# Performance work log

Hardware: AMD Instinct MI355X
Metric: run time of the kernel (lower is better)

Reference implementation:

```python
import jax, jax.numpy as jnp
import numpy as np

B, T, D, S, H = 1024, 365, 5, 27, 256


def setup_inputs() -> dict:
    key = jax.random.key(0)
    ks = jax.random.split(key, 12)
    sc = 0.05
    return {
        "x_dyn": jax.random.normal(ks[0], (B, T, D), dtype=jnp.float32),
        "x_stat": jax.random.normal(ks[1], (B, S), dtype=jnp.float32),
        "W_i": jax.random.normal(ks[2], (H, S), dtype=jnp.float32) * sc,
        "b_i": jnp.zeros((H,), dtype=jnp.float32),
        "W_f": jax.random.normal(ks[3], (H, D + H), dtype=jnp.float32) * sc,
        "b_f": jnp.zeros((H,), dtype=jnp.float32),
        "W_g": jax.random.normal(ks[4], (H, D + H), dtype=jnp.float32) * sc,
        "b_g": jnp.zeros((H,), dtype=jnp.float32),
        "W_o": jax.random.normal(ks[5], (H, D + H), dtype=jnp.float32) * sc,
        "b_o": jnp.zeros((H,), dtype=jnp.float32),
        "W_head": jax.random.normal(ks[6], (1, H), dtype=jnp.float32) * sc,
        "b_head": jnp.zeros((1,), dtype=jnp.float32),
    }


def _ealstm(x_dyn, x_stat, W_i, b_i, W_f, b_f, W_g, b_g, W_o, b_o, W_head, b_head):
    d = x_dyn.shape[-1]
    # static input gate (computed once, constant over time)
    i_gate = jax.nn.sigmoid(x_stat @ W_i.T + b_i)  # [B, H]
    # split concat-weights into dyn-input and hidden parts; precompute x projections
    W_fx, W_fh = W_f[:, :d], W_f[:, d:]
    W_gx, W_gh = W_g[:, :d], W_g[:, d:]
    W_ox, W_oh = W_o[:, :d], W_o[:, d:]
    pre_f = jnp.einsum("btd,hd->tbh", x_dyn, W_fx) + b_f  # [T, B, H]
    pre_g = jnp.einsum("btd,hd->tbh", x_dyn, W_gx) + b_g
    pre_o = jnp.einsum("btd,hd->tbh", x_dyn, W_ox) + b_o

    bsz = x_dyn.shape[0]
    h0 = jnp.zeros((bsz, W_f.shape[0]), dtype=x_dyn.dtype)
    c0 = jnp.zeros_like(h0)

    def step(carry, xs):
        h, c = carry
        pf, pg, po = xs
        f = jax.nn.sigmoid(pf + h @ W_fh.T)
        g = jnp.tanh(pg + h @ W_gh.T)
        o = jax.nn.sigmoid(po + h @ W_oh.T)
        c = f * c + i_gate * g
        h = o * jnp.tanh(c)
        return (h, c), None

    (h, _), _ = jax.lax.scan(step, (h0, c0), (pre_f, pre_g, pre_o))
    # dropout is identity in eval mode
    return h @ W_head.T + b_head  # [B, 1]


def reference(x_dyn, x_stat, W_i, b_i, W_f, b_f, W_g, b_g, W_o, b_o, W_head, b_head):
    return _ealstm(x_dyn, x_stat, W_i, b_i, W_f, b_f, W_g, b_g, W_o, b_o, W_head, b_head)
```

## Files before the change

kernel.cpp:

```cpp
#include <hip/hip_runtime.h>

#define HID      256
#define DDYN     5
#define NS       27
#define TS       365
#define BS       4
#define NW       8
#define UPW      32
#define NTILE    6
#define STRIDE_A 296
#define G3       768

typedef short short8 __attribute__((ext_vector_type(8)));
typedef float f32x4  __attribute__((ext_vector_type(4)));
typedef float f32x2  __attribute__((ext_vector_type(2)));

__device__ __forceinline__ unsigned short f2bf(float f) {
    union { float f; unsigned u; } v; v.f = f;
    unsigned r = v.u + 0x7FFFu + ((v.u >> 16) & 1u);
    return (unsigned short)(r >> 16);
}
__device__ __forceinline__ float fsig(float x) {
    float e = __builtin_amdgcn_exp2f(-1.4426950408889634f * x);
    return __builtin_amdgcn_rcpf(1.0f + e);
}
__device__ __forceinline__ float ftanh(float x) {
    float e = __builtin_amdgcn_exp2f(2.8853900817779268f * x);
    return 1.0f - 2.0f * __builtin_amdgcn_rcpf(1.0f + e);
}

__global__ __launch_bounds__(512, 2)
void ealstm_kernel(const float* __restrict__ x_dyn,  const float* __restrict__ x_stat,
                   const float* __restrict__ W_i,    const float* __restrict__ b_i,
                   const float* __restrict__ W_f,    const float* __restrict__ b_f,
                   const float* __restrict__ W_g,    const float* __restrict__ b_g,
                   const float* __restrict__ W_o,    const float* __restrict__ b_o,
                   const float* __restrict__ W_head, const float* __restrict__ b_head,
                   float* __restrict__ out)
{
    __shared__ __align__(16) unsigned short Abuf[2][16 * STRIDE_A];
    __shared__ __align__(16) float          pre[G3 * 4];
    __shared__ __align__(16) unsigned short WxL[G3 * 8];
    __shared__ __align__(16) unsigned short xc[TS * 20];
    __shared__ __align__(16) float          xst[BS * NS];

    const int tid  = threadIdx.x;
    const int bid  = blockIdx.x;
    const int b0   = bid * BS;
    const int lane = tid & 63;
    const int wv   = tid >> 6;
    const int q    = lane >> 4;
    const int n    = lane & 15;
    const int ul   = lane & 31;
    const int r0   = (lane >> 5) * 2;
    const int u    = wv * UPW + ul;

    for (int i = tid; i < 2 * 16 * STRIDE_A / 2; i += 512)
        ((unsigned int*)Abuf)[i] = 0u;
    for (int i = tid; i < BS * NS; i += 512)
        xst[i] = x_stat[(b0 + i / NS) * NS + (i % NS)];
    for (int i = tid; i < TS * BS * DDYN; i += 512) {
        int b  = i / (TS * DDYN);
        int rr = i - b * (TS * DDYN);
        int t  = rr / DDYN;
        int d  = rr - t * DDYN;
        xc[t * 20 + b * DDYN + d] =
            f2bf(x_dyn[(size_t)(b0 + b) * (TS * DDYN) + t * DDYN + d]);
    }
    for (int col = tid; col < G3; col += 512) {
        int gate = col >> 8, hc = col & 255;
        const float* Wg = gate == 0 ? W_f : (gate == 1 ? W_g : W_o);
        const float* bg = gate == 0 ? b_f : (gate == 1 ? b_g : b_o);
        #pragma unroll
        for (int d = 0; d < DDYN; d++) WxL[col * 8 + d] = f2bf(Wg[hc * (DDYN + HID) + d]);
        WxL[col * 8 + 5] = f2bf(bg[hc]);
        WxL[col * 8 + 6] = 0; WxL[col * 8 + 7] = 0;
    }
    __syncthreads();
    if (tid < 2 * BS) Abuf[tid >> 2][(tid & 3) * STRIDE_A + 261] = 0x3F80;
    if (tid < BS * DDYN) {
        int r = tid / DDYN, d = tid - r * DDYN;
        Abuf[0][r * STRIDE_A + 256 + d] = xc[r * DDYN + d];
    }

    short8 Bf[NTILE][8];
    #pragma unroll
    for (int j = 0; j < NTILE; j++) {
        int g = j >> 1;
        int urow = wv * UPW + (j & 1) * 16 + n;
        const float* Wg = g == 0 ? W_f : (g == 1 ? W_g : W_o);
        const float* wrow = Wg + urow * (DDYN + HID) + DDYN;
        #pragma unroll
        for (int c = 0; c < 8; c++) {
            int k0 = c * 32 + q * 8;
            short8 fr;
            #pragma unroll
            for (int e = 0; e < 8; e++) fr[e] = (short)f2bf(wrow[k0 + e]);
            Bf[j][c] = fr;
        }
    }

    float ig0, ig1, c0 = 0.f, c1 = 0.f, h0f = 0.f, h1f = 0.f;
    {
        float a0 = b_i[u], a1 = a0;
        for (int s = 0; s < NS; s++) {
            float w = W_i[u * NS + s];
            a0 += xst[r0 * NS + s] * w;
            a1 += xst[(r0 + 1) * NS + s] * w;
        }
        ig0 = fsig(a0); ig1 = fsig(a1);
    }
    const float whead = W_head[u];
    __syncthreads();

    const int aoff = n * STRIDE_A;
    const int pb   = (wv * 96 + ul) * 4 + r0;

    for (int t = 0; t < TS; t++) {
        const unsigned short* __restrict__ pA = Abuf[t & 1];
        unsigned short*       __restrict__ pB = Abuf[(t + 1) & 1];

        f32x4 acc[NTILE];
        #pragma unroll
        for (int j = 0; j < NTILE; j++) acc[j] = (f32x4){0.f, 0.f, 0.f, 0.f};
        #pragma unroll
        for (int c = 0; c < 8; c++) {
            short8 a = *(const short8*)&pA[aoff + c * 32 + q * 8];
            #pragma unroll
            for (int j = 0; j < NTILE; j++)
                acc[j] = __builtin_amdgcn_mfma_f32_16x16x32_bf16(a, Bf[j][c], acc[j], 0, 0, 0);
        }
        {
            short8 a8 = *(const short8*)&pA[aoff + 256 + q * 8];
            #pragma unroll
            for (int j = 0; j < NTILE; j++) {
                short8 b8 = {};
                if (q == 0) {
                    int col = (j >> 1) * 256 + wv * UPW + (j & 1) * 16 + n;
                    b8 = *(const short8*)&WxL[col * 8];
                }
                acc[j] = __builtin_amdgcn_mfma_f32_16x16x32_bf16(a8, b8, acc[j], 0, 0, 0);
            }
        }
        if (q == 0) {
            #pragma unroll
            for (int j = 0; j < NTILE; j++)
                *(f32x4*)&pre[(wv * 96 + (j >> 1) * 32 + (j & 1) * 16 + n) * 4] = acc[j];
        }
        __asm__ volatile("s_waitcnt lgkmcnt(0)" ::: "memory");

        f32x2 pf = *(const f32x2*)&pre[pb];
        f32x2 pg = *(const f32x2*)&pre[pb + 128];
        f32x2 po = *(const f32x2*)&pre[pb + 256];
        {
            float f  = fsig(pf[0]);
            float g_ = ftanh(pg[0]);
            float o  = fsig(po[0]);
            c0 = f * c0 + ig0 * g_;
            float h = o * ftanh(c0);
            pB[r0 * STRIDE_A + u] = f2bf(h);
            if (t == TS - 1) h0f = h;
        }
        {
            float f  = fsig(pf[1]);
            float g_ = ftanh(pg[1]);
            float o  = fsig(po[1]);
            c1 = f * c1 + ig1 * g_;
            float h = o * ftanh(c1);
            pB[(r0 + 1) * STRIDE_A + u] = f2bf(h);
            if (t == TS - 1) h1f = h;
        }
        if (t + 1 < TS && tid < BS * DDYN) {
            int r = tid / DDYN, d = tid - r * DDYN;
            pB[r * STRIDE_A + 256 + d] = xc[(t + 1) * 20 + tid];
        }
        __syncthreads();
    }

    pre[u * 4 + r0]     = h0f * whead;
    pre[u * 4 + r0 + 1] = h1f * whead;
    __syncthreads();
    if (tid < 64) {
        f32x4 s = *(const f32x4*)&pre[tid * 4];
        #pragma unroll
        for (int k = 1; k < 4; k++) {
            f32x4 v = *(const f32x4*)&pre[(tid + k * 64) * 4];
            #pragma unroll
            for (int r = 0; r < BS; r++) s[r] += v[r];
        }
        #pragma unroll
        for (int off = 32; off > 0; off >>= 1)
            #pragma unroll
            for (int r = 0; r < BS; r++) s[r] += __shfl_down(s[r], off, 64);
        if (tid == 0) {
            float bh = b_head[0];
            #pragma unroll
            for (int r = 0; r < BS; r++) out[b0 + r] = s[r] + bh;
        }
    }
}

extern "C" void kernel_launch(void* const* d_in, const int* in_sizes, int n_in,
                              void* d_out, int out_size, void* d_ws, size_t ws_size,
                              hipStream_t stream) {
    ealstm_kernel<<<256, 512, 0, stream>>>(
        (const float*)d_in[0],  (const float*)d_in[1],  (const float*)d_in[2],
        (const float*)d_in[3],  (const float*)d_in[4],  (const float*)d_in[5],
        (const float*)d_in[6],  (const float*)d_in[7],  (const float*)d_in[8],
        (const float*)d_in[9],  (const float*)d_in[10], (const float*)d_in[11],
        (float*)d_out);
}
```

Measured before the change: 707.9 us.

## Split LSTM recurrence across 16 waves with one unit-row per thread

Doubles the block to 1024 threads, so each of 16 waves owns 16 hidden units and 3 MFMA tiles instead of 32 units and 6 tiles. Each thread now updates a single (unit, batch-row) cell state. The aim is to shorten the serial per-timestep MFMA chain and gate math on the recurrence critical path. The cost is a barrier across 16 waves every step and tighter register limits per thread. The final hidden state is now read back from the bf16 shared buffer instead of being kept in fp32, a small precision change.

Measured after the change: 707.2 us. No clear change (-0.1%).

```diff
diff --git a/kernel.cpp b/kernel.cpp
--- a/kernel.cpp
+++ b/kernel.cpp
@@ -5,21 +5,24 @@
 #define NS       27
 #define TS       365
 #define BS       4
-#define NW       8
-#define UPW      32
-#define NTILE    6
+#define NW       16
+#define UPW      16
+#define NTILE    3
 #define STRIDE_A 296
 #define G3       768
 
 typedef short short8 __attribute__((ext_vector_type(8)));
 typedef float f32x4  __attribute__((ext_vector_type(4)));
-typedef float f32x2  __attribute__((ext_vector_type(2)));
 
 __device__ __forceinline__ unsigned short f2bf(float f) {
     union { float f; unsigned u; } v; v.f = f;
     unsigned r = v.u + 0x7FFFu + ((v.u >> 16) & 1u);
     return (unsigned short)(r >> 16);
 }
+__device__ __forceinline__ float bf2f(unsigned short s) {
+    union { unsigned u; float f; } v; v.u = ((unsigned)s) << 16;
+    return v.f;
+}
 __device__ __forceinline__ float fsig(float x) {
     float e = __builtin_amdgcn_exp2f(-1.4426950408889634f * x);
     return __builtin_amdgcn_rcpf(1.0f + e);
@@ -29,7 +32,7 @@
     return 1.0f - 2.0f * __builtin_amdgcn_rcpf(1.0f + e);
 }
 
-__global__ __launch_bounds__(512, 2)
+__global__ __launch_bounds__(1024)
 void ealstm_kernel(const float* __restrict__ x_dyn,  const float* __restrict__ x_stat,
                    const float* __restrict__ W_i,    const float* __restrict__ b_i,
                    const float* __restrict__ W_f,    const float* __restrict__ b_f,
@@ -39,7 +42,7 @@
                    float* __restrict__ out)
 {
     __shared__ __align__(16) unsigned short Abuf[2][16 * STRIDE_A];
-    __shared__ __align__(16) float          pre[G3 * 4];
+    __shared__ __align__(16) float          pre[NW * 192];
     __shared__ __align__(16) unsigned short WxL[G3 * 8];
     __shared__ __align__(16) unsigned short xc[TS * 20];
     __shared__ __align__(16) float          xst[BS * NS];
@@ -51,15 +54,15 @@
     const int wv   = tid >> 6;
     const int q    = lane >> 4;
     const int n    = lane & 15;
-    const int ul   = lane & 31;
-    const int r0   = (lane >> 5) * 2;
-    const int u    = wv * UPW + ul;
-
-    for (int i = tid; i < 2 * 16 * STRIDE_A / 2; i += 512)
+    const int up   = lane >> 2;
+    const int r    = lane & 3;
+    const int u    = wv * UPW + up;
+
+    for (int i = tid; i < 2 * 16 * STRIDE_A / 2; i += 1024)
         ((unsigned int*)Abuf)[i] = 0u;
-    for (int i = tid; i < BS * NS; i += 512)
+    for (int i = tid; i < BS * NS; i += 1024)
         xst[i] = x_stat[(b0 + i / NS) * NS + (i % NS)];
-    for (int i = tid; i < TS * BS * DDYN; i += 512) {
+    for (int i = tid; i < TS * BS * DDYN; i += 1024) {
         int b  = i / (TS * DDYN);
         int rr = i - b * (TS * DDYN);
         int t  = rr / DDYN;
@@ -67,7 +70,8 @@
         xc[t * 20 + b * DDYN + d] =
             f2bf(x_dyn[(size_t)(b0 + b) * (TS * DDYN) + t * DDYN + d]);
     }
-    for (int col = tid; col < G3; col += 512) {
+    if (tid < G3) {
+        int col = tid;
         int gate = col >> 8, hc = col & 255;
         const float* Wg = gate == 0 ? W_f : (gate == 1 ? W_g : W_o);
         const float* bg = gate == 0 ? b_f : (gate == 1 ? b_g : b_o);
@@ -79,16 +83,15 @@
     __syncthreads();
     if (tid < 2 * BS) Abuf[tid >> 2][(tid & 3) * STRIDE_A + 261] = 0x3F80;
     if (tid < BS * DDYN) {
-        int r = tid / DDYN, d = tid - r * DDYN;
-        Abuf[0][r * STRIDE_A + 256 + d] = xc[r * DDYN + d];
+        int rr = tid / DDYN, d = tid - rr * DDYN;
+        Abuf[0][rr * STRIDE_A + 256 + d] = xc[rr * DDYN + d];
     }
 
     short8 Bf[NTILE][8];
     #pragma unroll
     for (int j = 0; j < NTILE; j++) {
-        int g = j >> 1;
-        int urow = wv * UPW + (j & 1) * 16 + n;
-        const float* Wg = g == 0 ? W_f : (g == 1 ? W_g : W_o);
+        int urow = wv * UPW + n;
+        const float* Wg = j == 0 ? W_f : (j == 1 ? W_g : W_o);
         const float* wrow = Wg + urow * (DDYN + HID) + DDYN;
         #pragma unroll
         for (int c = 0; c < 8; c++) {
@@ -100,21 +103,17 @@
         }
     }
 
-    float ig0, ig1, c0 = 0.f, c1 = 0.f, h0f = 0.f, h1f = 0.f;
+    float ig, cst = 0.f;
     {
-        float a0 = b_i[u], a1 = a0;
-        for (int s = 0; s < NS; s++) {
-            float w = W_i[u * NS + s];
-            a0 += xst[r0 * NS + s] * w;
-            a1 += xst[(r0 + 1) * NS + s] * w;
-        }
-        ig0 = fsig(a0); ig1 = fsig(a1);
-    }
-    const float whead = W_head[u];
+        float a = b_i[u];
+        for (int s = 0; s < NS; s++)
+            a += xst[r * NS + s] * W_i[u * NS + s];
+        ig = fsig(a);
+    }
     __syncthreads();
 
     const int aoff = n * STRIDE_A;
-    const int pb   = (wv * 96 + ul) * 4 + r0;
+    const int pb   = wv * 192 + lane;
 
     for (int t = 0; t < TS; t++) {
         const unsigned short* __restrict__ pA = Abuf[t & 1];
@@ -135,50 +134,39 @@
             #pragma unroll
             for (int j = 0; j < NTILE; j++) {
                 short8 b8 = {};
-                if (q == 0) {
-                    int col = (j >> 1) * 256 + wv * UPW + (j & 1) * 16 + n;
-                    b8 = *(const short8*)&WxL[col * 8];
-                }
+                if (q == 0) b8 = *(const short8*)&WxL[(j * 256 + wv * UPW + n) * 8];
                 acc[j] = __builtin_amdgcn_mfma_f32_16x16x32_bf16(a8, b8, acc[j], 0, 0, 0);
             }
         }
         if (q == 0) {
             #pragma unroll
             for (int j = 0; j < NTILE; j++)
-                *(f32x4*)&pre[(wv * 96 + (j >> 1) * 32 + (j & 1) * 16 + n) * 4] = acc[j];
+                *(f32x4*)&pre[wv * 192 + j * 64 + n * 4] = acc[j];
         }
         __asm__ volatile("s_waitcnt lgkmcnt(0)" ::: "memory");
 
-        f32x2 pf = *(const f32x2*)&pre[pb];
-        f32x2 pg = *(const f32x2*)&pre[pb + 128];
-        f32x2 po = *(const f32x2*)&pre[pb + 256];
+        float pf = pre[pb];
+        float pg = pre[pb + 64];
+        float po = pre[pb + 128];
         {
-            float f  = fsig(pf[0]);
-            float g_ = ftanh(pg[0]);
-            float o  = fsig(po[0]);
-            c0 = f * c0 + ig0 * g_;
-            float h = o * ftanh(c0);
-            pB[r0 * STRIDE_A + u] = f2bf(h);
-            if (t == TS - 1) h0f = h;
-        }
-        {
-            float f  = fsig(pf[1]);
-            float g_ = ftanh(pg[1]);
-            float o  = fsig(po[1]);
-            c1 = f * c1 + ig1 * g_;
-            float h = o * ftanh(c1);
-            pB[(r0 + 1) * STRIDE_A + u] = f2bf(h);
-            if (t == TS - 1) h1f = h;
+            float f  = fsig(pf);
+            float g_ = ftanh(pg);
+            float o  = fsig(po);
+            cst = f * cst + ig * g_;
+            float h = o * ftanh(cst);
+            pB[r * STRIDE_A + u] = f2bf(h);
         }
         if (t + 1 < TS && tid < BS * DDYN) {
-            int r = tid / DDYN, d = tid - r * DDYN;
-            pB[r * STRIDE_A + 256 + d] = xc[(t + 1) * 20 + tid];
+            int rr = tid / DDYN, d = tid - rr * DDYN;
+            pB[rr * STRIDE_A + 256 + d] = xc[(t + 1) * 20 + tid];
         }
         __syncthreads();
     }
 
-    pre[u * 4 + r0]     = h0f * whead;
-    pre[u * 4 + r0 + 1] = h1f * whead;
+    {
+        float h = bf2f(Abuf[1][r * STRIDE_A + u]);
+        pre[u * 4 + r] = h * W_head[u];
+    }
     __syncthreads();
     if (tid < 64) {
         f32x4 s = *(const f32x4*)&pre[tid * 4];
@@ -186,16 +174,16 @@
         for (int k = 1; k < 4; k++) {
             f32x4 v = *(const f32x4*)&pre[(tid + k * 64) * 4];
             #pragma unroll
-            for (int r = 0; r < BS; r++) s[r] += v[r];
+            for (int rr = 0; rr < BS; rr++) s[rr] += v[rr];
         }
         #pragma unroll
         for (int off = 32; off > 0; off >>= 1)
             #pragma unroll
-            for (int r = 0; r < BS; r++) s[r] += __shfl_down(s[r], off, 64);
+            for (int rr = 0; rr < BS; rr++) s[rr] += __shfl_down(s[rr], off, 64);
         if (tid == 0) {
             float bh = b_head[0];
             #pragma unroll
-            for (int r = 0; r < BS; r++) out[b0 + r] = s[r] + bh;
+            for (int rr = 0; rr < BS; rr++) out[b0 + rr] = s[rr] + bh;
         }
     }
 }
@@ -203,7 +191,7 @@
 extern "C" void kernel_launch(void* const* d_in, const int* in_sizes, int n_in,
                               void* d_out, int out_size, void* d_ws, size_t ws_size,
                               hipStream_t stream) {
-    ealstm_kernel<<<256, 512, 0, stream>>>(
+    ealstm_kernel<<<256, 1024, 0, stream>>>(
         (const float*)d_in[0],  (const float*)d_in[1],  (const float*)d_in[2],
         (const float*)d_in[3],  (const float*)d_in[4],  (const float*)d_in[5],
         (const float*)d_in[6],  (const float*)d_in[7],  (const float*)d_in[8],
```
